# Kernel optimization log

Measured on AMD Instinct MI355X. Metric: run time of the kernel, lower is better.

Reference implementation:

```python
import jax, jax.numpy as jnp
import numpy as np

N_NODES = 50000
N_EDGES = 800000
IN_F = 128
OUT_F = 128
EDGE_F = 6


def setup_inputs() -> dict:
    key = jax.random.key(0)
    k1, k2, k3, k4, k5, k6, k7 = jax.random.split(key, 7)
    nodeFeatures = jax.random.normal(k1, (N_NODES, IN_F), dtype=jnp.float32)
    edgeIndex = jax.random.randint(k2, (N_EDGES, 2), 0, N_NODES, dtype=jnp.int64)
    edgeFeatures = jax.random.normal(k3, (N_EDGES, EDGE_F), dtype=jnp.float32)
    # nn.Linear params (kaiming-uniform-ish init scale)
    lim_n = 1.0 / np.sqrt(IN_F)
    lim_e = 1.0 / np.sqrt(EDGE_F)
    W = jax.random.uniform(k4, (IN_F, OUT_F), minval=-lim_n, maxval=lim_n, dtype=jnp.float32)
    b = jax.random.uniform(k5, (OUT_F,), minval=-lim_n, maxval=lim_n, dtype=jnp.float32)
    We = jax.random.uniform(k6, (EDGE_F, OUT_F), minval=-lim_e, maxval=lim_e, dtype=jnp.float32)
    be = jax.random.uniform(k7, (OUT_F,), minval=-lim_e, maxval=lim_e, dtype=jnp.float32)
    return {"nodeFeatures": nodeFeatures, "edgeIndex": edgeIndex,
            "edgeFeatures": edgeFeatures, "W": W, "b": b, "We": We, "be": be}


def reference(nodeFeatures, edgeIndex, edgeFeatures, W, b, We, be):
    # node linear: [N, out]
    transformed = nodeFeatures @ W + b
    # edge linear: [E, out]
    edgeMsg = edgeFeatures @ We + be
    src = edgeIndex[:, 0]
    dst = edgeIndex[:, 1]
    # per-edge message = transformed[src] + edgeMsg, scatter-add into dst
    messages = transformed[src] + edgeMsg  # [E, out]
    aggregated = jax.ops.segment_sum(messages, dst, num_segments=nodeFeatures.shape[0])
    return jax.nn.relu(aggregated)
```

## Files before the change

### kernel.cpp

```cpp
#include <hip/hip_runtime.h>
#include <hip/hip_bf16.h>
#include <stdint.h>

#define IN_F 128
#define EDGE_F 6

using bf16x8 = __attribute__((ext_vector_type(8))) short;
using f32x4  = __attribute__((ext_vector_type(4))) float;

__device__ __forceinline__ float bf2f(unsigned short u) {
    return __uint_as_float(((unsigned int)u) << 16);
}
__device__ __forceinline__ unsigned short f2bfbits(float f) {
    __hip_bfloat16 h = __float2bfloat16(f);
    return *reinterpret_cast<unsigned short*>(&h);
}
__device__ __forceinline__ unsigned int packbf(float a, float b) {
    return ((unsigned int)f2bfbits(b) << 16) | (unsigned int)f2bfbits(a);
}

__global__ __launch_bounds__(256) void hist_cast(
        const int* __restrict__ eidx, const float* __restrict__ ef,
        int* __restrict__ cnt, int* __restrict__ rank,
        uint4* __restrict__ efp, int n_edges,
        const float* __restrict__ nf, unsigned short* __restrict__ nfb,
        int n_cast) {
    const int t = blockIdx.x * 256 + threadIdx.x;
    if (t < n_edges) {
        const int2 pr = reinterpret_cast<const int2*>(eidx)[t];
        const float2* efs = reinterpret_cast<const float2*>(ef + (size_t)t * EDGE_F);
        const float2 f0 = efs[0], f1 = efs[1], f2 = efs[2];
        uint4 q;
        q.x = (unsigned int)pr.x;
        q.y = packbf(f0.x, f0.y);
        q.z = packbf(f1.x, f1.y);
        q.w = packbf(f2.x, f2.y);
        efp[t] = q;
        rank[t] = atomicAdd(&cnt[pr.y], 1);
    }
    const int stride = gridDim.x * 256;
    for (int i = t; i < n_cast; i += stride) {
        const float4 lo = reinterpret_cast<const float4*>(nf)[2 * i];
        const float4 hi = reinterpret_cast<const float4*>(nf)[2 * i + 1];
        uint4 o;
        o.x = packbf(lo.x, lo.y); o.y = packbf(lo.z, lo.w);
        o.z = packbf(hi.x, hi.y); o.w = packbf(hi.z, hi.w);
        reinterpret_cast<uint4*>(nfb)[i] = o;
    }
}

__global__ __launch_bounds__(256) void scan_fused(
        const int* __restrict__ cnt, int* __restrict__ rowptr, int n, int nblk,
        unsigned long long* __restrict__ agg,
        const float* __restrict__ W, const float* __restrict__ b,
        const float* __restrict__ We, const float* __restrict__ be,
        unsigned short* __restrict__ Wpack, float* __restrict__ W2pack) {
    const int tid = threadIdx.x;
    const int blk = blockIdx.x;
    if (blk == nblk) {
        for (int idx = tid; idx < 16384; idx += 256) {
            int j = idx & 7, lane = (idx >> 3) & 63, ft = (idx >> 9) & 7, kb = idx >> 12;
            int k = kb * 32 + (lane >> 4) * 8 + j;
            int f = ft * 16 + (lane & 15);
            Wpack[idx] = f2bfbits(W[k * 128 + f]);
        }
        for (int idx = tid; idx < 1024; idx += 256) {
            int j = idx >> 7, f = idx & 127;
            float w = 0.f;
            if (j < 6)       w = We[j * 128 + f];
            else if (j == 6) w = b[f] + be[f];
            W2pack[idx] = w;
        }
        return;
    }
    __shared__ int sh[256];
    const int idx = blk * 256 + tid;
    const int v = (idx < n) ? cnt[idx] : 0;
    sh[tid] = v;
    __syncthreads();
    for (int off = 1; off < 256; off <<= 1) {
        int t2 = (tid >= off) ? sh[tid - off] : 0;
        __syncthreads();
        sh[tid] += t2;
        __syncthreads();
    }
    const int incl = sh[tid];
    if (tid == 0)
        atomicExch(&agg[blk], (1ULL << 32) | (unsigned int)sh[255]);
    int pre = 0;
    if (tid < blk) {
        unsigned long long x;
        do { x = atomicAdd(&agg[tid], 0ULL); } while ((x >> 32) == 0);
        pre = (int)(unsigned int)x;
    }
    __syncthreads();
    sh[tid] = pre;
    __syncthreads();
    for (int off = 128; off > 0; off >>= 1) {
        if (tid < off) sh[tid] += sh[tid + off];
        __syncthreads();
    }
    const int off0 = sh[0];
    if (idx < n) rowptr[idx] = off0 + incl - v;
    if (blk == nblk - 1 && tid == 255) rowptr[n] = off0 + incl;
}

__global__ __launch_bounds__(256) void fill_csr(
        const int* __restrict__ eidx, const int* __restrict__ rowptr,
        const int* __restrict__ rank, const uint4* __restrict__ efp,
        uint4* __restrict__ rec, int n_edges) {
    int e = blockIdx.x * 256 + threadIdx.x;
    if (e >= n_edges) return;
    const int dst = reinterpret_cast<const int2*>(eidx)[e].y;
    const int pos = rowptr[dst] + rank[e];
    rec[pos] = efp[e];
}

__global__ __launch_bounds__(256) void aggregate_bf16(
        const unsigned short* __restrict__ nfb, const uint4* __restrict__ rec,
        const int* __restrict__ rowptr, unsigned short* __restrict__ S,
        unsigned short* __restrict__ E8, int n_nodes) {
    const int lane = threadIdx.x & 63;
    const int wv = __builtin_amdgcn_readfirstlane(threadIdx.x >> 6);
    const int n = blockIdx.x * 4 + wv;
    if (n >= n_nodes) return;
    const int r0 = rowptr[n], r1 = rowptr[n + 1];
    const int deg = r1 - r0;
    float ax = 0.f, ay = 0.f;
    float e0 = 0.f, e1 = 0.f, e2 = 0.f, e3 = 0.f, e4 = 0.f, e5 = 0.f;
    int i = r0;
    for (; i + 3 < r1; i += 4) {
        const uint4 q0 = rec[i], q1 = rec[i + 1], q2 = rec[i + 2], q3 = rec[i + 3];
        const unsigned int u0 = reinterpret_cast<const unsigned int*>(nfb + (size_t)(int)q0.x * IN_F)[lane];
        const unsigned int u1 = reinterpret_cast<const unsigned int*>(nfb + (size_t)(int)q1.x * IN_F)[lane];
        const unsigned int u2 = reinterpret_cast<const unsigned int*>(nfb + (size_t)(int)q2.x * IN_F)[lane];
        const unsigned int u3 = reinterpret_cast<const unsigned int*>(nfb + (size_t)(int)q3.x * IN_F)[lane];
        ax += (bf2f((unsigned short)u0) + bf2f((unsigned short)u1))
            + (bf2f((unsigned short)u2) + bf2f((unsigned short)u3));
        ay += (bf2f((unsigned short)(u0 >> 16)) + bf2f((unsigned short)(u1 >> 16)))
            + (bf2f((unsigned short)(u2 >> 16)) + bf2f((unsigned short)(u3 >> 16)));
        e0 += (bf2f((unsigned short)q0.y) + bf2f((unsigned short)q1.y))
            + (bf2f((unsigned short)q2.y) + bf2f((unsigned short)q3.y));
        e1 += (bf2f((unsigned short)(q0.y >> 16)) + bf2f((unsigned short)(q1.y >> 16)))
            + (bf2f((unsigned short)(q2.y >> 16)) + bf2f((unsigned short)(q3.y >> 16)));
        e2 += (bf2f((unsigned short)q0.z) + bf2f((unsigned short)q1.z))
            + (bf2f((unsigned short)q2.z) + bf2f((unsigned short)q3.z));
        e3 += (bf2f((unsigned short)(q0.z >> 16)) + bf2f((unsigned short)(q1.z >> 16)))
            + (bf2f((unsigned short)(q2.z >> 16)) + bf2f((unsigned short)(q3.z >> 16)));
        e4 += (bf2f((unsigned short)q0.w) + bf2f((unsigned short)q1.w))
            + (bf2f((unsigned short)q2.w) + bf2f((unsigned short)q3.w));
        e5 += (bf2f((unsigned short)(q0.w >> 16)) + bf2f((unsigned short)(q1.w >> 16)))
            + (bf2f((unsigned short)(q2.w >> 16)) + bf2f((unsigned short)(q3.w >> 16)));
    }
    for (; i < r1; ++i) {
        const uint4 q0 = rec[i];
        const unsigned int u0 = reinterpret_cast<const unsigned int*>(nfb + (size_t)(int)q0.x * IN_F)[lane];
        ax += bf2f((unsigned short)u0); ay += bf2f((unsigned short)(u0 >> 16));
        e0 += bf2f((unsigned short)q0.y); e1 += bf2f((unsigned short)(q0.y >> 16));
        e2 += bf2f((unsigned short)q0.z); e3 += bf2f((unsigned short)(q0.z >> 16));
        e4 += bf2f((unsigned short)q0.w); e5 += bf2f((unsigned short)(q0.w >> 16));
    }
    unsigned short* row = S + (size_t)n * IN_F;
    reinterpret_cast<unsigned int*>(row)[lane] = packbf(ax, ay);
    if (lane == 0) {
        uint4 q;
        q.x = packbf(e0, e1);
        q.y = packbf(e2, e3);
        q.z = packbf(e4, e5);
        q.w = packbf((float)deg, 0.f);
        *reinterpret_cast<uint4*>(E8 + (size_t)n * 8) = q;
    }
}

__global__ __launch_bounds__(256) void gemm_mfma(
        const unsigned short* __restrict__ S, const unsigned short* __restrict__ E8,
        const unsigned short* __restrict__ Wpack, const float* __restrict__ W2pack,
        float* __restrict__ out, int n_nodes) {
    __shared__ __align__(16) short Wl[16384];
    __shared__ float W2l[1024];
    const int tid = threadIdx.x;
    for (int i = tid; i < 2048; i += 256)
        reinterpret_cast<uint4*>(Wl)[i] = reinterpret_cast<const uint4*>(Wpack)[i];
    for (int i = tid; i < 1024; i += 256) W2l[i] = W2pack[i];

    const int wv = tid >> 6, lane = tid & 63;
    const int m = lane & 15, quad = lane >> 4;
    const int n0 = blockIdx.x * 64 + wv * 16;

    const int arow = min(n0 + m, n_nodes - 1);
    const unsigned short* ap = S + (size_t)arow * IN_F + quad * 8;
    bf16x8 a[4];
#pragma unroll
    for (int kb = 0; kb < 4; ++kb)
        a[kb] = *reinterpret_cast<const bf16x8*>(ap + kb * 32);

    __syncthreads();

    f32x4 acc[8];
#pragma unroll
    for (int ft = 0; ft < 8; ++ft) acc[ft] = (f32x4){0.f, 0.f, 0.f, 0.f};

#pragma unroll
    for (int kb = 0; kb < 4; ++kb) {
#pragma unroll
        for (int ft = 0; ft < 8; ++ft) {
            const bf16x8 bfrag =
                reinterpret_cast<const bf16x8*>(Wl)[(kb * 8 + ft) * 64 + lane];
            acc[ft] = __builtin_amdgcn_mfma_f32_16x16x32_bf16(a[kb], bfrag, acc[ft], 0, 0, 0);
        }
    }

    float e[4][7];
#pragma unroll
    for (int r = 0; r < 4; ++r) {
        const int n = min(n0 + quad * 4 + r, n_nodes - 1);
        const uint4 q = *reinterpret_cast<const uint4*>(E8 + (size_t)n * 8);
        e[r][0] = bf2f((unsigned short)q.x); e[r][1] = bf2f((unsigned short)(q.x >> 16));
        e[r][2] = bf2f((unsigned short)q.y); e[r][3] = bf2f((unsigned short)(q.y >> 16));
        e[r][4] = bf2f((unsigned short)q.z); e[r][5] = bf2f((unsigned short)(q.z >> 16));
        e[r][6] = bf2f((unsigned short)q.w);
    }
#pragma unroll
    for (int ft = 0; ft < 8; ++ft) {
        const int f = ft * 16 + m;
        float w2[7];
#pragma unroll
        for (int j = 0; j < 7; ++j) w2[j] = W2l[j * 128 + f];
#pragma unroll
        for (int r = 0; r < 4; ++r) {
            const int n = n0 + quad * 4 + r;
            if (n < n_nodes) {
                float v = acc[ft][r];
#pragma unroll
                for (int j = 0; j < 7; ++j) v += e[r][j] * w2[j];
                out[(size_t)n * 128 + f] = fmaxf(v, 0.f);
            }
        }
    }
}

extern "C" void kernel_launch(void* const* d_in, const int* in_sizes, int n_in,
                              void* d_out, int out_size, void* d_ws, size_t ws_size,
                              hipStream_t stream) {
    const float* nf = (const float*)d_in[0];
    const int* eidx = (const int*)d_in[1];
    const float* ef = (const float*)d_in[2];
    const float* W  = (const float*)d_in[3];
    const float* b  = (const float*)d_in[4];
    const float* We = (const float*)d_in[5];
    const float* be = (const float*)d_in[6];
    float* out = (float*)d_out;

    const int n_nodes = in_sizes[0] / IN_F;
    const int n_edges = in_sizes[1] / 2;

    uint4* rec = (uint4*)d_ws;
    uint4* efp = rec + n_edges;
    unsigned short* S = (unsigned short*)(efp + n_edges);
    unsigned short* E8 = S + (size_t)n_nodes * IN_F;
    unsigned short* Wpack = E8 + (size_t)n_nodes * 8;
    float* W2pack = (float*)(Wpack + 16384);
    int* cnt = (int*)(W2pack + 1024);
    unsigned long long* agg = (unsigned long long*)(cnt + n_nodes);
    int* rowptr = (int*)(agg + 256);
    int* rank   = rowptr + n_nodes + 1;
    unsigned short* nfb = (unsigned short*)(rank + n_edges);

    hipMemsetAsync(cnt, 0, (size_t)n_nodes * 4 + 256 * 8, stream);

    const int eb = (n_edges + 255) / 256;
    const int nblk = (n_nodes + 255) / 256;
    const int n_cast = n_nodes * (IN_F / 8);

    hist_cast<<<eb, 256, 0, stream>>>(eidx, ef, cnt, rank, efp, n_edges, nf, nfb, n_cast);
    scan_fused<<<nblk + 1, 256, 0, stream>>>(cnt, rowptr, n_nodes, nblk, agg,
                                             W, b, We, be, Wpack, W2pack);
    fill_csr<<<eb, 256, 0, stream>>>(eidx, rowptr, rank, efp, rec, n_edges);

    aggregate_bf16<<<(n_nodes + 3) / 4, 256, 0, stream>>>(nfb, rec, rowptr, S, E8, n_nodes);
    gemm_mfma<<<(n_nodes + 63) / 64, 256, 0, stream>>>(S, E8, Wpack, W2pack, out, n_nodes);
}
```

Measured before the change: 209.9 us.

## Fuse CSR build and aggregation into one cooperative persistent kernel

Replaces the memset and four separate launches (histogram/cast, scan, CSR fill, aggregation) with a single cooperative kernel that uses grid-wide syncs between phases and grid-stride loops. The aim is to remove per-launch overhead and the idle gaps between small dependent kernels. In exchange the grid is capped by occupancy, so the gather-heavy aggregation runs with fewer resident waves in a persistent loop. The grid syncs add their own cost, and the cross-block scan spin-wait relies on all scan blocks being co-resident.

After: 639.7 us. +204.8%, slower.

```diff
diff --git a/kernel.cpp b/kernel.cpp
--- a/kernel.cpp
+++ b/kernel.cpp
@@ -1,9 +1,12 @@
 #include <hip/hip_runtime.h>
+#include <hip/hip_cooperative_groups.h>
 #include <hip/hip_bf16.h>
 #include <stdint.h>
 
 #define IN_F 128
 #define EDGE_F 6
+
+namespace cg = cooperative_groups;
 
 using bf16x8 = __attribute__((ext_vector_type(8))) short;
 using f32x4  = __attribute__((ext_vector_type(4))) float;
@@ -19,27 +22,41 @@
     return ((unsigned int)f2bfbits(b) << 16) | (unsigned int)f2bfbits(a);
 }
 
-__global__ __launch_bounds__(256) void hist_cast(
+__global__ __launch_bounds__(256, 8) void fused_front(
         const int* __restrict__ eidx, const float* __restrict__ ef,
+        const float* __restrict__ nf,
+        const float* __restrict__ W, const float* __restrict__ b,
+        const float* __restrict__ We, const float* __restrict__ be,
         int* __restrict__ cnt, int* __restrict__ rank,
-        uint4* __restrict__ efp, int n_edges,
-        const float* __restrict__ nf, unsigned short* __restrict__ nfb,
-        int n_cast) {
-    const int t = blockIdx.x * 256 + threadIdx.x;
-    if (t < n_edges) {
-        const int2 pr = reinterpret_cast<const int2*>(eidx)[t];
-        const float2* efs = reinterpret_cast<const float2*>(ef + (size_t)t * EDGE_F);
+        uint4* __restrict__ efp, unsigned short* __restrict__ nfb,
+        int* __restrict__ rowptr, unsigned long long* __restrict__ agg,
+        unsigned short* __restrict__ Wpack, float* __restrict__ W2pack,
+        uint4* __restrict__ rec, unsigned short* __restrict__ S,
+        unsigned short* __restrict__ E8,
+        int n_nodes, int n_edges, int nscan) {
+    cg::grid_group grid = cg::this_grid();
+    __shared__ int sh[256];
+    const int tid = threadIdx.x, blk = blockIdx.x;
+    const int gt = blk * 256 + tid;
+    const int gs = gridDim.x * 256;
+
+    for (int i = gt; i < n_nodes + 512; i += gs) cnt[i] = 0;
+    grid.sync();
+
+    for (int e = gt; e < n_edges; e += gs) {
+        const int2 pr = reinterpret_cast<const int2*>(eidx)[e];
+        const float2* efs = reinterpret_cast<const float2*>(ef + (size_t)e * EDGE_F);
         const float2 f0 = efs[0], f1 = efs[1], f2 = efs[2];
         uint4 q;
         q.x = (unsigned int)pr.x;
         q.y = packbf(f0.x, f0.y);
         q.z = packbf(f1.x, f1.y);
         q.w = packbf(f2.x, f2.y);
-        efp[t] = q;
-        rank[t] = atomicAdd(&cnt[pr.y], 1);
-    }
-    const int stride = gridDim.x * 256;
-    for (int i = t; i < n_cast; i += stride) {
+        efp[e] = q;
+        rank[e] = atomicAdd(&cnt[pr.y], 1);
+    }
+    const int n_cast = n_nodes * (IN_F / 8);
+    for (int i = gt; i < n_cast; i += gs) {
         const float4 lo = reinterpret_cast<const float4*>(nf)[2 * i];
         const float4 hi = reinterpret_cast<const float4*>(nf)[2 * i + 1];
         uint4 o;
@@ -47,17 +64,39 @@
         o.z = packbf(hi.x, hi.y); o.w = packbf(hi.z, hi.w);
         reinterpret_cast<uint4*>(nfb)[i] = o;
     }
-}
-
-__global__ __launch_bounds__(256) void scan_fused(
-        const int* __restrict__ cnt, int* __restrict__ rowptr, int n, int nblk,
-        unsigned long long* __restrict__ agg,
-        const float* __restrict__ W, const float* __restrict__ b,
-        const float* __restrict__ We, const float* __restrict__ be,
-        unsigned short* __restrict__ Wpack, float* __restrict__ W2pack) {
-    const int tid = threadIdx.x;
-    const int blk = blockIdx.x;
-    if (blk == nblk) {
+    grid.sync();
+
+    if (blk < nscan) {
+        const int idx = blk * 256 + tid;
+        const int v = (idx < n_nodes) ? cnt[idx] : 0;
+        sh[tid] = v;
+        __syncthreads();
+        for (int off = 1; off < 256; off <<= 1) {
+            int t2 = (tid >= off) ? sh[tid - off] : 0;
+            __syncthreads();
+            sh[tid] += t2;
+            __syncthreads();
+        }
+        const int incl = sh[tid];
+        if (tid == 0)
+            atomicExch(&agg[blk], (1ULL << 32) | (unsigned int)sh[255]);
+        int pre = 0;
+        if (tid < blk) {
+            unsigned long long x;
+            do { x = atomicAdd(&agg[tid], 0ULL); } while ((x >> 32) == 0);
+            pre = (int)(unsigned int)x;
+        }
+        __syncthreads();
+        sh[tid] = pre;
+        __syncthreads();
+        for (int off = 128; off > 0; off >>= 1) {
+            if (tid < off) sh[tid] += sh[tid + off];
+            __syncthreads();
+        }
+        const int off0 = sh[0];
+        if (idx < n_nodes) rowptr[idx] = off0 + incl - v;
+        if (blk == nscan - 1 && tid == 255) rowptr[n_nodes] = off0 + incl;
+    } else if (blk == nscan) {
         for (int idx = tid; idx < 16384; idx += 256) {
             int j = idx & 7, lane = (idx >> 3) & 63, ft = (idx >> 9) & 7, kb = idx >> 12;
             int k = kb * 32 + (lane >> 4) * 8 + j;
@@ -71,104 +110,63 @@
             else if (j == 6) w = b[f] + be[f];
             W2pack[idx] = w;
         }
-        return;
-    }
-    __shared__ int sh[256];
-    const int idx = blk * 256 + tid;
-    const int v = (idx < n) ? cnt[idx] : 0;
-    sh[tid] = v;
-    __syncthreads();
-    for (int off = 1; off < 256; off <<= 1) {
-        int t2 = (tid >= off) ? sh[tid - off] : 0;
-        __syncthreads();
-        sh[tid] += t2;
-        __syncthreads();
-    }
-    const int incl = sh[tid];
-    if (tid == 0)
-        atomicExch(&agg[blk], (1ULL << 32) | (unsigned int)sh[255]);
-    int pre = 0;
-    if (tid < blk) {
-        unsigned long long x;
-        do { x = atomicAdd(&agg[tid], 0ULL); } while ((x >> 32) == 0);
-        pre = (int)(unsigned int)x;
-    }
-    __syncthreads();
-    sh[tid] = pre;
-    __syncthreads();
-    for (int off = 128; off > 0; off >>= 1) {
-        if (tid < off) sh[tid] += sh[tid + off];
-        __syncthreads();
-    }
-    const int off0 = sh[0];
-    if (idx < n) rowptr[idx] = off0 + incl - v;
-    if (blk == nblk - 1 && tid == 255) rowptr[n] = off0 + incl;
-}
-
-__global__ __launch_bounds__(256) void fill_csr(
-        const int* __restrict__ eidx, const int* __restrict__ rowptr,
-        const int* __restrict__ rank, const uint4* __restrict__ efp,
-        uint4* __restrict__ rec, int n_edges) {
-    int e = blockIdx.x * 256 + threadIdx.x;
-    if (e >= n_edges) return;
-    const int dst = reinterpret_cast<const int2*>(eidx)[e].y;
-    const int pos = rowptr[dst] + rank[e];
-    rec[pos] = efp[e];
-}
-
-__global__ __launch_bounds__(256) void aggregate_bf16(
-        const unsigned short* __restrict__ nfb, const uint4* __restrict__ rec,
-        const int* __restrict__ rowptr, unsigned short* __restrict__ S,
-        unsigned short* __restrict__ E8, int n_nodes) {
-    const int lane = threadIdx.x & 63;
-    const int wv = __builtin_amdgcn_readfirstlane(threadIdx.x >> 6);
-    const int n = blockIdx.x * 4 + wv;
-    if (n >= n_nodes) return;
-    const int r0 = rowptr[n], r1 = rowptr[n + 1];
-    const int deg = r1 - r0;
-    float ax = 0.f, ay = 0.f;
-    float e0 = 0.f, e1 = 0.f, e2 = 0.f, e3 = 0.f, e4 = 0.f, e5 = 0.f;
-    int i = r0;
-    for (; i + 3 < r1; i += 4) {
-        const uint4 q0 = rec[i], q1 = rec[i + 1], q2 = rec[i + 2], q3 = rec[i + 3];
-        const unsigned int u0 = reinterpret_cast<const unsigned int*>(nfb + (size_t)(int)q0.x * IN_F)[lane];
-        const unsigned int u1 = reinterpret_cast<const unsigned int*>(nfb + (size_t)(int)q1.x * IN_F)[lane];
-        const unsigned int u2 = reinterpret_cast<const unsigned int*>(nfb + (size_t)(int)q2.x * IN_F)[lane];
-        const unsigned int u3 = reinterpret_cast<const unsigned int*>(nfb + (size_t)(int)q3.x * IN_F)[lane];
-        ax += (bf2f((unsigned short)u0) + bf2f((unsigned short)u1))
-            + (bf2f((unsigned short)u2) + bf2f((unsigned short)u3));
-        ay += (bf2f((unsigned short)(u0 >> 16)) + bf2f((unsigned short)(u1 >> 16)))
-            + (bf2f((unsigned short)(u2 >> 16)) + bf2f((unsigned short)(u3 >> 16)));
-        e0 += (bf2f((unsigned short)q0.y) + bf2f((unsigned short)q1.y))
-            + (bf2f((unsigned short)q2.y) + bf2f((unsigned short)q3.y));
-        e1 += (bf2f((unsigned short)(q0.y >> 16)) + bf2f((unsigned short)(q1.y >> 16)))
-            + (bf2f((unsigned short)(q2.y >> 16)) + bf2f((unsigned short)(q3.y >> 16)));
-        e2 += (bf2f((unsigned short)q0.z) + bf2f((unsigned short)q1.z))
-            + (bf2f((unsigned short)q2.z) + bf2f((unsigned short)q3.z));
-        e3 += (bf2f((unsigned short)(q0.z >> 16)) + bf2f((unsigned short)(q1.z >> 16)))
-            + (bf2f((unsigned short)(q2.z >> 16)) + bf2f((unsigned short)(q3.z >> 16)));
-        e4 += (bf2f((unsigned short)q0.w) + bf2f((unsigned short)q1.w))
-            + (bf2f((unsigned short)q2.w) + bf2f((unsigned short)q3.w));
-        e5 += (bf2f((unsigned short)(q0.w >> 16)) + bf2f((unsigned short)(q1.w >> 16)))
-            + (bf2f((unsigned short)(q2.w >> 16)) + bf2f((unsigned short)(q3.w >> 16)));
-    }
-    for (; i < r1; ++i) {
-        const uint4 q0 = rec[i];
-        const unsigned int u0 = reinterpret_cast<const unsigned int*>(nfb + (size_t)(int)q0.x * IN_F)[lane];
-        ax += bf2f((unsigned short)u0); ay += bf2f((unsigned short)(u0 >> 16));
-        e0 += bf2f((unsigned short)q0.y); e1 += bf2f((unsigned short)(q0.y >> 16));
-        e2 += bf2f((unsigned short)q0.z); e3 += bf2f((unsigned short)(q0.z >> 16));
-        e4 += bf2f((unsigned short)q0.w); e5 += bf2f((unsigned short)(q0.w >> 16));
-    }
-    unsigned short* row = S + (size_t)n * IN_F;
-    reinterpret_cast<unsigned int*>(row)[lane] = packbf(ax, ay);
-    if (lane == 0) {
-        uint4 q;
-        q.x = packbf(e0, e1);
-        q.y = packbf(e2, e3);
-        q.z = packbf(e4, e5);
-        q.w = packbf((float)deg, 0.f);
-        *reinterpret_cast<uint4*>(E8 + (size_t)n * 8) = q;
+    }
+    grid.sync();
+
+    for (int e = gt; e < n_edges; e += gs) {
+        const int dst = reinterpret_cast<const int2*>(eidx)[e].y;
+        rec[rowptr[dst] + rank[e]] = efp[e];
+    }
+    grid.sync();
+
+    const int lane = tid & 63;
+    const int nwaves = gridDim.x * 4;
+    for (int n = blk * 4 + (tid >> 6); n < n_nodes; n += nwaves) {
+        const int r0 = rowptr[n], r1 = rowptr[n + 1];
+        const int deg = r1 - r0;
+        float ax = 0.f, ay = 0.f;
+        float e0 = 0.f, e1 = 0.f, e2 = 0.f, e3 = 0.f, e4 = 0.f, e5 = 0.f;
+        int i = r0;
+        for (; i + 3 < r1; i += 4) {
+            const uint4 q0 = rec[i], q1 = rec[i + 1], q2 = rec[i + 2], q3 = rec[i + 3];
+            const unsigned int u0 = reinterpret_cast<const unsigned int*>(nfb + (size_t)(int)q0.x * IN_F)[lane];
+            const unsigned int u1 = reinterpret_cast<const unsigned int*>(nfb + (size_t)(int)q1.x * IN_F)[lane];
+            const unsigned int u2 = reinterpret_cast<const unsigned int*>(nfb + (size_t)(int)q2.x * IN_F)[lane];
+            const unsigned int u3 = reinterpret_cast<const unsigned int*>(nfb + (size_t)(int)q3.x * IN_F)[lane];
+            ax += (bf2f((unsigned short)u0) + bf2f((unsigned short)u1))
+                + (bf2f((unsigned short)u2) + bf2f((unsigned short)u3));
+            ay += (bf2f((unsigned short)(u0 >> 16)) + bf2f((unsigned short)(u1 >> 16)))
+                + (bf2f((unsigned short)(u2 >> 16)) + bf2f((unsigned short)(u3 >> 16)));
+            e0 += (bf2f((unsigned short)q0.y) + bf2f((unsigned short)q1.y))
+                + (bf2f((unsigned short)q2.y) + bf2f((unsigned short)q3.y));
+            e1 += (bf2f((unsigned short)(q0.y >> 16)) + bf2f((unsigned short)(q1.y >> 16)))
+                + (bf2f((unsigned short)(q2.y >> 16)) + bf2f((unsigned short)(q3.y >> 16)));
+            e2 += (bf2f((unsigned short)q0.z) + bf2f((unsigned short)q1.z))
+                + (bf2f((unsigned short)q2.z) + bf2f((unsigned short)q3.z));
+            e3 += (bf2f((unsigned short)(q0.z >> 16)) + bf2f((unsigned short)(q1.z >> 16)))
+                + (bf2f((unsigned short)(q2.z >> 16)) + bf2f((unsigned short)(q3.z >> 16)));
+            e4 += (bf2f((unsigned short)q0.w) + bf2f((unsigned short)q1.w))
+                + (bf2f((unsigned short)q2.w) + bf2f((unsigned short)q3.w));
+            e5 += (bf2f((unsigned short)(q0.w >> 16)) + bf2f((unsigned short)(q1.w >> 16)))
+                + (bf2f((unsigned short)(q2.w >> 16)) + bf2f((unsigned short)(q3.w >> 16)));
+        }
+        for (; i < r1; ++i) {
+            const uint4 q0 = rec[i];
+            const unsigned int u0 = reinterpret_cast<const unsigned int*>(nfb + (size_t)(int)q0.x * IN_F)[lane];
+            ax += bf2f((unsigned short)u0); ay += bf2f((unsigned short)(u0 >> 16));
+            e0 += bf2f((unsigned short)q0.y); e1 += bf2f((unsigned short)(q0.y >> 16));
+            e2 += bf2f((unsigned short)q0.z); e3 += bf2f((unsigned short)(q0.z >> 16));
+            e4 += bf2f((unsigned short)q0.w); e5 += bf2f((unsigned short)(q0.w >> 16));
+        }
+        reinterpret_cast<unsigned int*>(S + (size_t)n * IN_F)[lane] = packbf(ax, ay);
+        if (lane == 0) {
+            uint4 q;
+            q.x = packbf(e0, e1);
+            q.y = packbf(e2, e3);
+            q.z = packbf(e4, e5);
+            q.w = packbf((float)deg, 0.f);
+            *reinterpret_cast<uint4*>(E8 + (size_t)n * 8) = q;
+        }
     }
 }
 
@@ -242,8 +240,8 @@
 extern "C" void kernel_launch(void* const* d_in, const int* in_sizes, int n_in,
                               void* d_out, int out_size, void* d_ws, size_t ws_size,
                               hipStream_t stream) {
+    const int* eidx = (const int*)d_in[1];
     const float* nf = (const float*)d_in[0];
-    const int* eidx = (const int*)d_in[1];
     const float* ef = (const float*)d_in[2];
     const float* W  = (const float*)d_in[3];
     const float* b  = (const float*)d_in[4];
@@ -266,17 +264,23 @@
     int* rank   = rowptr + n_nodes + 1;
     unsigned short* nfb = (unsigned short*)(rank + n_edges);
 
-    hipMemsetAsync(cnt, 0, (size_t)n_nodes * 4 + 256 * 8, stream);
-
-    const int eb = (n_edges + 255) / 256;
-    const int nblk = (n_nodes + 255) / 256;
-    const int n_cast = n_nodes * (IN_F / 8);
-
-    hist_cast<<<eb, 256, 0, stream>>>(eidx, ef, cnt, rank, efp, n_edges, nf, nfb, n_cast);
-    scan_fused<<<nblk + 1, 256, 0, stream>>>(cnt, rowptr, n_nodes, nblk, agg,
-                                             W, b, We, be, Wpack, W2pack);
-    fill_csr<<<eb, 256, 0, stream>>>(eidx, rowptr, rank, efp, rec, n_edges);
-
-    aggregate_bf16<<<(n_nodes + 3) / 4, 256, 0, stream>>>(nfb, rec, rowptr, S, E8, n_nodes);
+    const int nscan = (n_nodes + 255) / 256;
+
+    int maxb = 8;
+    hipOccupancyMaxActiveBlocksPerMultiprocessor(&maxb, fused_front, 256, 0);
+    if (maxb < 1) maxb = 1;
+    int grid = maxb * 256;
+    if (grid > 2048) grid = 2048;
+
+    void* args[] = {
+        (void*)&eidx, (void*)&ef, (void*)&nf, (void*)&W, (void*)&b,
+        (void*)&We, (void*)&be, (void*)&cnt, (void*)&rank, (void*)&efp,
+        (void*)&nfb, (void*)&rowptr, (void*)&agg, (void*)&Wpack,
+        (void*)&W2pack, (void*)&rec, (void*)&S, (void*)&E8,
+        (void*)&n_nodes, (void*)&n_edges, (void*)&nscan
+    };
+    hipLaunchCooperativeKernel((const void*)fused_front, dim3(grid), dim3(256),
+                               args, 0, stream);
+
     gemm_mfma<<<(n_nodes + 63) / 64, 256, 0, stream>>>(S, E8, Wpack, W2pack, out, n_nodes);
 }
```
